# Performance work log

Measured on AMD Instinct MI355X. Metric: run time of the kernel, lower is better.

Reference implementation:

```python
import jax, jax.numpy as jnp
import numpy as np

H = 16; KV = 4; D = 128; HID = 2048; MAX_POS = 4096; RANK = 8; ALPHA = 16.0; THETA = 10000.0


def _lora_dense(x, kernel, a, b):
    # base kernel path is stop-gradient'd in the original LoRADense
    x = x.astype(jnp.bfloat16)
    y = x @ jax.lax.stop_gradient(kernel.astype(jnp.bfloat16))
    y = y + (ALPHA / RANK) * ((x @ a.astype(jnp.bfloat16)) @ b.astype(jnp.bfloat16))
    return y.astype(jnp.float32)


def _apply_rope(xq, xk, position_ids):
    # complex rotation expressed with real cos/sin on interleaved (even, odd) pairs
    dt = xq.dtype
    xq = xq.astype(jnp.bfloat16).astype(jnp.float32)
    xk = xk.astype(jnp.bfloat16).astype(jnp.float32)
    d = xq.shape[-1]
    inv_freq = 1.0 / THETA ** (jnp.arange(0, d, 2)[: d // 2].astype(jnp.float32) / d)
    angles = jnp.arange(MAX_POS, dtype=jnp.float32)[:, None] * inv_freq[None, :]  # (max_pos, d/2)
    cos = jnp.cos(angles)[position_ids][:, :, None, :]  # (b, s, 1, d/2)
    sin = jnp.sin(angles)[position_ids][:, :, None, :]

    def rot(x):
        xe = x[..., 0::2]
        xo = x[..., 1::2]
        re = xe * cos - xo * sin
        im = xe * sin + xo * cos
        return jnp.stack((re, im), axis=-1).reshape(x.shape)

    return rot(xq).astype(dt), rot(xk).astype(dt)


def _forward(hidden_states, attention_mask, position_ids, wq_kernel, wq_a, wq_b,
             wk_kernel, wk_a, wk_b, wv_kernel, wv_a, wv_b, wo_kernel, wo_a, wo_b):
    b, s, _ = hidden_states.shape
    hs = hidden_states.astype(jnp.bfloat16)
    xq = _lora_dense(hs, wq_kernel, wq_a, wq_b).reshape(b, s, H, D)
    g = H // KV
    # GQA: repeat each kv head g times along the head axis ('b s (h d) -> b s (h g) d')
    xk = jnp.repeat(_lora_dense(hs, wk_kernel, wk_a, wk_b).reshape(b, s, KV, D), g, axis=2)
    xv = jnp.repeat(_lora_dense(hs, wv_kernel, wv_a, wv_b).reshape(b, s, KV, D), g, axis=2)
    xq, xk = _apply_rope(xq, xk, position_ids)
    causal = jnp.tril(jnp.ones((s, s), dtype=bool))
    mask = attention_mask[:, None, None, :] & causal[None, None]  # (b, 1, q, k)
    bias = jnp.where(mask, 0.0, jnp.finfo(jnp.float32).min)
    scale = 1.0 / np.sqrt(D).astype(np.float32)
    scores = jnp.einsum('bqhd,bkhd->bhqk', (xq * scale).astype(jnp.bfloat16),
                        xk.astype(jnp.bfloat16)).astype(jnp.float32) + bias
    attn = jax.nn.softmax(scores, axis=-1)
    out = jnp.einsum('bhqk,bkhd->bqhd', attn, xv).reshape(b, s, H * D)
    return _lora_dense(out, wo_kernel, wo_a, wo_b)


def setup_inputs():
    key = jax.random.key(0)
    ks = jax.random.split(key, 16)
    B, S = 2, 2048
    w = lambda k, shp, sc=0.02: jax.random.normal(k, shp, dtype=jnp.float32) * sc
    return {
        'hidden_states': jax.random.normal(ks[0], (B, S, HID), dtype=jnp.float32),
        'attention_mask': jnp.ones((B, S), dtype=bool),
        'position_ids': jnp.broadcast_to(jnp.arange(S, dtype=jnp.int32), (B, S)),
        'wq_kernel': w(ks[1], (HID, H * D)),
        'wq_a': w(ks[2], (HID, RANK), 0.01),
        'wq_b': w(ks[3], (RANK, H * D), 0.01),
        'wk_kernel': w(ks[4], (HID, KV * D)),
        'wk_a': w(ks[5], (HID, RANK), 0.01),
        'wk_b': w(ks[6], (RANK, KV * D), 0.01),
        'wv_kernel': w(ks[7], (HID, KV * D)),
        'wv_a': w(ks[8], (HID, RANK), 0.01),
        'wv_b': w(ks[9], (RANK, KV * D), 0.01),
        'wo_kernel': w(ks[10], (H * D, HID)),
        'wo_a': w(ks[11], (H * D, RANK), 0.01),
        'wo_b': w(ks[12], (RANK, HID), 0.01),
    }


def reference(hidden_states, attention_mask, position_ids, wq_kernel, wq_a, wq_b,
              wk_kernel, wk_a, wk_b, wv_kernel, wv_a, wv_b, wo_kernel, wo_a, wo_b):
    return _forward(hidden_states, attention_mask, position_ids, wq_kernel, wq_a, wq_b,
                    wk_kernel, wk_a, wk_b, wv_kernel, wv_a, wv_b, wo_kernel, wo_a, wo_b)
```

## Files before the change

kernel.cpp:

```cpp
#include <hip/hip_runtime.h>
#include <hip/hip_bf16.h>
#include <cstdint>

#define H_    16
#define KV_   4
#define D_    128
#define HID_  2048
#define B_    2
#define S_    2048
#define NROW_ (B_*S_)
#define HD_   (H_*D_)
#define KVD_  (KV_*D_)
#define NQKV_ (HD_ + 2*KVD_)
#define SCALE_ 0.08838834764831843f
#define NEG_  -1e30f

typedef float  f32x4  __attribute__((ext_vector_type(4)));
typedef __bf16 bf16x8 __attribute__((ext_vector_type(8)));
typedef __bf16 bf16x4 __attribute__((ext_vector_type(4)));

__device__ __forceinline__ unsigned short f2bf(float x) {
  unsigned u = __float_as_uint(x);
  return (unsigned short)((u + 0x7FFFu + ((u >> 16) & 1u)) >> 16);
}
__device__ __forceinline__ float bf2f(unsigned short h) {
  return __uint_as_float(((unsigned)h) << 16);
}

__device__ __forceinline__ void glds16(const void* g, void* l) {
  typedef __attribute__((address_space(1))) const char G;
  typedef __attribute__((address_space(3))) char L;
  __builtin_amdgcn_global_load_lds((const G*)(unsigned long long)g,
                                   (L*)(unsigned)(unsigned long long)l, 16, 0, 0);
}

__global__ __launch_bounds__(256) void fold_w2(const float* __restrict__ W,
                                               const float* __restrict__ A,
                                               const float* __restrict__ Bm,
                                               unsigned short* __restrict__ Wt,
                                               int K, int N) {
  __shared__ float Bs[8 * 64];
  __shared__ unsigned short tt[64 * 72];
  const int tid = threadIdx.x;
  const int k0 = blockIdx.x << 6, n0 = blockIdx.y << 6;
#pragma unroll
  for (int i = 0; i < 2; ++i) {
    int c = i * 256 + tid;
    Bs[c] = bf2f(f2bf(Bm[(c >> 6) * N + n0 + (c & 63)]));
  }
  __syncthreads();
  const int kr = tid >> 2, nc = (tid & 3) << 4;
  float a[8];
#pragma unroll
  for (int r = 0; r < 8; ++r) a[r] = 2.0f * bf2f(f2bf(A[(k0 + kr) * 8 + r]));
#pragma unroll
  for (int i = 0; i < 4; ++i) {
    float4 wv = *(const float4*)(W + (size_t)(k0 + kr) * N + n0 + nc + i * 4);
    float e[4] = {wv.x, wv.y, wv.z, wv.w};
#pragma unroll
    for (int q = 0; q < 4; ++q) {
      int n = nc + i * 4 + q;
      float acc = bf2f(f2bf(e[q]));
#pragma unroll
      for (int r = 0; r < 8; ++r) acc += a[r] * Bs[r * 64 + n];
      tt[kr * 72 + n] = f2bf(acc);
    }
  }
  __syncthreads();
  const int nr = tid >> 2, kc = (tid & 3) << 4;
#pragma unroll
  for (int i = 0; i < 2; ++i) {
    unsigned short o[8];
#pragma unroll
    for (int e2 = 0; e2 < 8; ++e2) o[e2] = tt[(kc + i * 8 + e2) * 72 + nr];
    *(bf16x8*)(Wt + (size_t)(n0 + nr) * K + k0 + kc + i * 8) = *(const bf16x8*)o;
  }
}

__global__ __launch_bounds__(256) void cast_x(const float* __restrict__ in,
                                              unsigned short* __restrict__ out, int n4) {
  int i = blockIdx.x * 256 + threadIdx.x;
  if (i >= n4) return;
  float4 v = ((const float4*)in)[i];
  ushort4 o; o.x = f2bf(v.x); o.y = f2bf(v.y); o.z = f2bf(v.z); o.w = f2bf(v.w);
  ((ushort4*)out)[i] = o;
}

__global__ void trig_k(float* __restrict__ tab) {
  int p = blockIdx.x, j = threadIdx.x;
  float invf = __powf(10000.0f, -(float)j / 64.0f);
  float a = (float)p * invf;
  float s, c;
  sincosf(a, &s, &c);
  tab[(p * 64 + j) * 2 + 0] = c;
  tab[(p * 64 + j) * 2 + 1] = s;
}

__global__ __launch_bounds__(256) void rope2(unsigned short* __restrict__ QKV,
                                             const int* __restrict__ pos,
                                             const float* __restrict__ trig) {
  int gid = blockIdx.x * 256 + threadIdx.x;
  int row = gid / 160;
  int ch = gid - row * 160;
  bool isq = ch < 128;
  int col = isq ? (ch << 4) : (HD_ + ((ch - 128) << 4));
  int j0 = (isq ? (ch & 7) : ((ch - 128) & 7)) << 3;
  int pp = pos[row];
  const float* tb = trig + ((size_t)pp * 64 + j0) * 2;
  float4 t0 = *(const float4*)(tb);
  float4 t1 = *(const float4*)(tb + 4);
  float4 t2 = *(const float4*)(tb + 8);
  float4 t3 = *(const float4*)(tb + 12);
  float cc[8] = {t0.x, t0.z, t1.x, t1.z, t2.x, t2.z, t3.x, t3.z};
  float ss[8] = {t0.y, t0.w, t1.y, t1.w, t2.y, t2.w, t3.y, t3.w};
  unsigned short* base = QKV + (size_t)row * NQKV_ + col;
  unsigned short xin[16], xo[16];
  *(bf16x8*)xin = *(const bf16x8*)base;
  *(bf16x8*)(xin + 8) = *(const bf16x8*)(base + 8);
  float scl = isq ? SCALE_ : 1.0f;
#pragma unroll
  for (int p = 0; p < 8; ++p) {
    float x0 = bf2f(xin[2 * p]), x1 = bf2f(xin[2 * p + 1]);
    float re = (x0 * cc[p] - x1 * ss[p]) * scl;
    float im = (x0 * ss[p] + x1 * cc[p]) * scl;
    xo[2 * p] = f2bf(re); xo[2 * p + 1] = f2bf(im);
  }
  *(bf16x8*)base = *(const bf16x8*)xo;
  *(bf16x8*)(base + 8) = *(const bf16x8*)(xo + 8);
}

__global__ __launch_bounds__(256) void vtrans_k(const unsigned short* __restrict__ QKV,
                                                unsigned short* __restrict__ VT) {
  __shared__ unsigned short t[64 * 65];
  const int tid = threadIdx.x;
  const int s0 = blockIdx.x << 6, d0 = blockIdx.y << 6;
  const int bk = blockIdx.z, b = bk >> 2, hkv = bk & 3;
#pragma unroll
  for (int i = 0; i < 2; ++i) {
    int c = i * 256 + tid;
    int sr = c >> 3, c8 = c & 7;
    bf16x8 v = *(const bf16x8*)(QKV + (size_t)(b * S_ + s0 + sr) * NQKV_
                                + HD_ + KVD_ + hkv * D_ + d0 + c8 * 8);
    const unsigned short* u = (const unsigned short*)&v;
#pragma unroll
    for (int k = 0; k < 8; ++k) t[sr * 65 + c8 * 8 + k] = u[k];
  }
  __syncthreads();
#pragma unroll
  for (int i = 0; i < 2; ++i) {
    int c = i * 256 + tid;
    int dr = c >> 3, c8 = c & 7;
    unsigned short o[8];
#pragma unroll
    for (int k = 0; k < 8; ++k) o[k] = t[(c8 * 8 + k) * 65 + dr];
    *(bf16x8*)(VT + ((size_t)(bk * 128 + d0 + dr)) * S_ + s0 + c8 * 8) =
        *(const bf16x8*)o;
  }
}

template <int BN, int OUTF32>
__global__ __launch_bounds__(512, 1) void gemm256(const unsigned short* __restrict__ A,
                                                  const unsigned short* __restrict__ Bt,
                                                  void* __restrict__ C,
                                                  int M, int N, int K) {
  constexpr int ASLAB = 256 * 32;
  constexpr int BSLAB = BN * 32;
  constexpr int BUFE = 2 * ASLAB + 2 * BSLAB;
  constexpr int NFR = BN / 64;
  constexpr int WCOL = BN / 4;
  constexpr int VMN = 2 + BN / 128;
  __shared__ __align__(16) unsigned short lds[2 * BUFE];
  const int tid = threadIdx.x, lane = tid & 63, w = tid >> 6;
  const int g = lane >> 4, l15 = lane & 15;
  const int wm = w >> 2, wn = w & 3;

  const int nbn = N / BN;
  const int cpx = gridDim.x >> 3;
  const int sw = (blockIdx.x & 7) * cpx + (blockIdx.x >> 3);
  const int bm = sw / nbn, bn = sw - bm * nbn;
  const int row0 = bm << 8, col0 = bn * BN;

  auto stageA = [&](int kt, int kh, int buf) {
#pragma unroll
    for (int i = 0; i < 2; ++i) {
      int L = (i * 8 + w) * 64 + lane;
      int r = L >> 2, c = L & 3;
      int sc = c ^ ((r >> 1) & 3);
      glds16(A + (size_t)(row0 + r) * K + (kt << 6) + kh * 32 + sc * 8,
             (char*)lds + (size_t)(buf * BUFE + kh * ASLAB) * 2 + (size_t)(i * 8 + w) * 1024);
    }
  };
  auto stageB = [&](int kt, int kh, int buf) {
#pragma unroll
    for (int i = 0; i < BN / 128; ++i) {
      int L = (i * 8 + w) * 64 + lane;
      int r = L >> 2, c = L & 3;
      int sc = c ^ ((r >> 1) & 3);
      glds16(Bt + (size_t)(col0 + r) * K + (kt << 6) + kh * 32 + sc * 8,
             (char*)lds + (size_t)(buf * BUFE + 2 * ASLAB + kh * BSLAB) * 2 + (size_t)(i * 8 + w) * 1024);
    }
  };

  f32x4 acc[8][NFR];
#pragma unroll
  for (int i = 0; i < 8; ++i)
#pragma unroll
    for (int j = 0; j < NFR; ++j) acc[i][j] = (f32x4){0.f, 0.f, 0.f, 0.f};

  bf16x8 af[4], bfr[NFR];
  auto rdA = [&](int buf, int kh, int mh) {
#pragma unroll
    for (int mi = 0; mi < 4; ++mi) {
      int r = wm * 128 + mh * 64 + mi * 16 + l15;
      int cc = g ^ ((r >> 1) & 3);
      af[mi] = *(const bf16x8*)(lds + buf * BUFE + kh * ASLAB + r * 32 + cc * 8);
    }
  };
  auto rdB = [&](int buf, int kh) {
#pragma unroll
    for (int ni = 0; ni < NFR; ++ni) {
      int r = wn * WCOL + ni * 16 + l15;
      int cc = g ^ ((r >> 1) & 3);
      bfr[ni] = *(const bf16x8*)(lds + buf * BUFE + 2 * ASLAB + kh * BSLAB + r * 32 + cc * 8);
    }
  };
  auto domfma = [&](int mh) {
    __builtin_amdgcn_s_setprio(1);
#pragma unroll
    for (int mi = 0; mi < 4; ++mi)
#pragma unroll
      for (int ni = 0; ni < NFR; ++ni)
        acc[mh * 4 + mi][ni] =
            __builtin_amdgcn_mfma_f32_16x16x32_bf16(af[mi], bfr[ni], acc[mh * 4 + mi][ni], 0, 0, 0);
    __builtin_amdgcn_s_setprio(0);
  };

  stageA(0, 0, 0); stageB(0, 0, 0); stageA(0, 1, 0); stageB(0, 1, 0);
  asm volatile("s_waitcnt vmcnt(0)" ::: "memory");
  __builtin_amdgcn_s_barrier();

  const int nkt = K >> 6;
  for (int kt = 0; kt < nkt; ++kt) {
    const int buf = kt & 1, nb = buf ^ 1;
    const bool more = kt + 1 < nkt;
    rdA(buf, 0, 0); rdB(buf, 0);
    if (more) stageA(kt + 1, 0, nb);
    __builtin_amdgcn_s_barrier();
    domfma(0);
    __builtin_amdgcn_s_barrier();
    rdA(buf, 0, 1);
    if (more) {
      stageB(kt + 1, 0, nb);
      asm volatile("s_waitcnt vmcnt(%0)" :: "i"(VMN) : "memory");
    } else {
      asm volatile("s_waitcnt vmcnt(0)" ::: "memory");
    }
    __builtin_amdgcn_s_barrier();
    domfma(1);
    __builtin_amdgcn_s_barrier();
    rdA(buf, 1, 0); rdB(buf, 1);
    if (more) stageA(kt + 1, 1, nb);
    __builtin_amdgcn_s_barrier();
    domfma(0);
    __builtin_amdgcn_s_barrier();
    rdA(buf, 1, 1);
    if (more) {
      stageB(kt + 1, 1, nb);
      asm volatile("s_waitcnt vmcnt(%0)" :: "i"(VMN) : "memory");
    }
    __builtin_amdgcn_s_barrier();
    domfma(1);
    __builtin_amdgcn_s_barrier();
  }

#pragma unroll
  for (int mi8 = 0; mi8 < 8; ++mi8)
#pragma unroll
    for (int jj = 0; jj < 4; ++jj) {
      int r = row0 + wm * 128 + mi8 * 16 + g * 4 + jj;
#pragma unroll
      for (int ni = 0; ni < NFR; ++ni) {
        int cc = col0 + wn * WCOL + ni * 16 + l15;
        float v = acc[mi8][ni][jj];
        if (OUTF32) {
          ((float*)C)[(size_t)r * N + cc] = v;
        } else {
          __bf16 e = (__bf16)v;
          ((unsigned short*)C)[(size_t)r * N + cc] = *(unsigned short*)&e;
        }
      }
    }
}

__global__ __launch_bounds__(256) void attn_k(const unsigned short* __restrict__ QKV,
                                              const unsigned short* __restrict__ VT,
                                              unsigned short* __restrict__ O) {
  __shared__ __align__(16) unsigned short lK[2][64 * 128];
  __shared__ __align__(16) unsigned short lV[2][128 * 64];
  __shared__ __align__(16) unsigned short lP[4][16 * 72];
  const int tid = threadIdx.x, lane = tid & 63, w = tid >> 6;
  const int g = lane >> 4, l15 = lane & 15;

  const int dd = blockIdx.x;
  const int grp = dd & 7;
  const int t64 = dd >> 3;
  const int pair = t64 & 15;
  const int bh = grp * 4 + (t64 >> 4);
  const int b = bh >> 4, h = bh & 15, hkv = (h >> 2);

  auto stage = [&](int kb, int bsel) {
#pragma unroll
    for (int i = 0; i < 4; ++i) {
      int cbase = i * 256 + w * 64;
      int c = cbase + lane;
      { int r = c >> 4, p = c & 15, lc = p ^ (r & 7);
        glds16(QKV + (size_t)(b * S_ + kb + r) * NQKV_ + HD_ + hkv * D_ + lc * 8,
               (char*)(&lK[bsel][0]) + (size_t)cbase * 16); }
      { int d = c >> 3, p = c & 7, lc = p ^ (d & 7);
        glds16(VT + ((size_t)((b * 4 + hkv) * 128 + d)) * S_ + kb + lc * 8,
               (char*)(&lV[bsel][0]) + (size_t)cbase * 16); }
    }
  };

  for (int qsel = 0; qsel < 2; ++qsel) {
    const int qt = qsel ? (31 - pair) : pair;
    const int q_base = qt << 6;
    const int ntile = qt + 1;

    bf16x8 qf[4];
#pragma unroll
    for (int ks = 0; ks < 4; ++ks)
      qf[ks] = *(const bf16x8*)(QKV + (size_t)(b * S_ + q_base + w * 16 + l15) * NQKV_
                                + h * D_ + ks * 32 + g * 8);

    f32x4 oacc[8];
#pragma unroll
    for (int nd = 0; nd < 8; ++nd) oacc[nd] = (f32x4){0.f, 0.f, 0.f, 0.f};
    float mrun = NEG_, lrun = 0.f;

    stage(0, 0);
    __syncthreads();
    int cur = 0;
    for (int t = 0; t < ntile; ++t) {
      if (t + 1 < ntile) stage((t + 1) << 6, cur ^ 1);

      const unsigned short* Kb = &lK[cur][0];
      const unsigned short* Vb = &lV[cur][0];

      f32x4 sacc[4];
#pragma unroll
      for (int m = 0; m < 4; ++m) sacc[m] = (f32x4){0.f, 0.f, 0.f, 0.f};
      __builtin_amdgcn_s_setprio(1);
#pragma unroll
      for (int ks = 0; ks < 4; ++ks) {
        bf16x8 kf[4];
#pragma unroll
        for (int m = 0; m < 4; ++m) {
          int r = m * 16 + l15;
          int lc = (ks * 4 + g) ^ (r & 7);
          kf[m] = *(const bf16x8*)(Kb + r * 128 + lc * 8);
        }
#pragma unroll
        for (int m = 0; m < 4; ++m)
          sacc[m] = __builtin_amdgcn_mfma_f32_16x16x32_bf16(kf[m], qf[ks], sacc[m], 0, 0, 0);
      }
      __builtin_amdgcn_s_setprio(0);

      if (t == qt) {
#pragma unroll
        for (int m = 0; m < 4; ++m)
#pragma unroll
          for (int jj = 0; jj < 4; ++jj)
            if (m * 16 + g * 4 + jj > w * 16 + l15) sacc[m][jj] = NEG_;
      }

      float pm = NEG_;
#pragma unroll
      for (int m = 0; m < 4; ++m)
#pragma unroll
        for (int jj = 0; jj < 4; ++jj) pm = fmaxf(pm, sacc[m][jj]);
      pm = fmaxf(pm, __shfl_xor(pm, 16));
      pm = fmaxf(pm, __shfl_xor(pm, 32));
      bool skip = __all(pm <= mrun + 8.f);
      float mnew = skip ? mrun : fmaxf(mrun, pm);
      float ls = 0.f;
#pragma unroll
      for (int m = 0; m < 4; ++m)
#pragma unroll
        for (int jj = 0; jj < 4; ++jj) {
          float pv = __expf(sacc[m][jj] - mnew);
          sacc[m][jj] = pv;
          ls += pv;
        }
      ls += __shfl_xor(ls, 16);
      ls += __shfl_xor(ls, 32);
      if (skip) {
        lrun += ls;
      } else {
        float sc = __expf(mrun - mnew);
        lrun = lrun * sc + ls;
        mrun = mnew;
#pragma unroll
        for (int jj = 0; jj < 4; ++jj) {
          int srcl = (lane & 48) | (g * 4 + jj);
          float s = __shfl(sc, srcl);
#pragma unroll
          for (int nd = 0; nd < 8; ++nd) oacc[nd][jj] *= s;
        }
      }

#pragma unroll
      for (int m = 0; m < 4; ++m) {
        bf16x4 pk = {(__bf16)sacc[m][0], (__bf16)sacc[m][1],
                     (__bf16)sacc[m][2], (__bf16)sacc[m][3]};
        *(bf16x4*)(&lP[w][0] + l15 * 72 + m * 16 + g * 4) = pk;
      }

      __builtin_amdgcn_s_setprio(1);
#pragma unroll
      for (int ks = 0; ks < 2; ++ks) {
        bf16x8 pf = *(const bf16x8*)(&lP[w][0] + l15 * 72 + ks * 32 + g * 8);
#pragma unroll
        for (int nd = 0; nd < 8; ++nd) {
          int d = nd * 16 + l15;
          int lc = (ks * 4 + g) ^ (d & 7);
          bf16x8 vf = *(const bf16x8*)(Vb + d * 64 + lc * 8);
          oacc[nd] = __builtin_amdgcn_mfma_f32_16x16x32_bf16(pf, vf, oacc[nd], 0, 0, 0);
        }
      }
      __builtin_amdgcn_s_setprio(0);
      __syncthreads();
      cur ^= 1;
    }

    float inv[4];
#pragma unroll
    for (int jj = 0; jj < 4; ++jj) {
      int srcl = (lane & 48) | (g * 4 + jj);
      inv[jj] = 1.0f / __shfl(lrun, srcl);
    }
    unsigned short* sE = &lK[0][0];
#pragma unroll
    for (int nd = 0; nd < 8; ++nd)
#pragma unroll
      for (int jj = 0; jj < 4; ++jj) {
        __bf16 e = (__bf16)(oacc[nd][jj] * inv[jj]);
        sE[(w * 16 + g * 4 + jj) * 136 + nd * 16 + l15] = *(unsigned short*)&e;
      }
    __syncthreads();
#pragma unroll
    for (int i = 0; i < 4; ++i) {
      int c = i * 256 + tid;
      int r = c >> 4, c16 = c & 15;
      bf16x8 vv = *(const bf16x8*)(sE + r * 136 + c16 * 8);
      *(bf16x8*)(O + (size_t)(b * S_ + q_base + r) * HD_ + h * D_ + c16 * 8) = vv;
    }
    __syncthreads();
  }
}

extern "C" void kernel_launch(void* const* d_in, const int* in_sizes, int n_in,
                              void* d_out, int out_size, void* d_ws, size_t ws_size,
                              hipStream_t stream) {
  const float* hs  = (const float*)d_in[0];
  const int*   pos = (const int*)d_in[2];
  const float* wq  = (const float*)d_in[3];
  const float* wqa = (const float*)d_in[4];
  const float* wqb = (const float*)d_in[5];
  const float* wk  = (const float*)d_in[6];
  const float* wka = (const float*)d_in[7];
  const float* wkb = (const float*)d_in[8];
  const float* wv  = (const float*)d_in[9];
  const float* wva = (const float*)d_in[10];
  const float* wvb = (const float*)d_in[11];
  const float* wo  = (const float*)d_in[12];
  const float* woa = (const float*)d_in[13];
  const float* wob = (const float*)d_in[14];

  char* ws = (char*)d_ws;
  unsigned short* Xb   = (unsigned short*)(ws);
  unsigned short* Wqkv = (unsigned short*)(ws + 16777216);
  unsigned short* Wot  = (unsigned short*)(ws + 29360128);
  unsigned short* QKV  = (unsigned short*)(ws + 37748736);
  unsigned short* VT   = (unsigned short*)(ws + 62914560);
  float*          trig = (float*)(ws + 67108864);

  fold_w2<<<dim3(32, 32), 256, 0, stream>>>(wq, wqa, wqb, Wqkv, 2048, 2048);
  fold_w2<<<dim3(32, 8),  256, 0, stream>>>(wk, wka, wkb, Wqkv + (size_t)2048 * 2048, 2048, 512);
  fold_w2<<<dim3(32, 8),  256, 0, stream>>>(wv, wva, wvb, Wqkv + (size_t)2560 * 2048, 2048, 512);
  fold_w2<<<dim3(32, 32), 256, 0, stream>>>(wo, woa, wob, Wot, 2048, 2048);
  cast_x<<<8192, 256, 0, stream>>>(hs, Xb, 2097152);
  trig_k<<<4096, 64, 0, stream>>>(trig);
  gemm256<256, 0><<<192, 512, 0, stream>>>(Xb, Wqkv, QKV, 4096, 3072, 2048);
  rope2<<<2560, 256, 0, stream>>>(QKV, pos, trig);
  vtrans_k<<<dim3(32, 2, 8), 256, 0, stream>>>(QKV, VT);
  attn_k<<<512, 256, 0, stream>>>(QKV, VT, Xb );
  gemm256<128, 1><<<256, 512, 0, stream>>>(Xb, Wot, d_out, 4096, 2048, 2048);
}
```

Baseline: 213.6 us.

## Fuse RoPE into QKV GEMM epilogue and unroll attention loop with static buffers

Removes the standalone RoPE kernel by applying the rotation and query scaling inside the QKV GEMM store epilogue, using a lane-pair shuffle and the trig table. The attention kernel is restructured into a manually two-way unrolled loop over a single shared buffer with precomputed global and LDS offsets, removing dynamic buffer indexing. The trig table is shrunk to cover only the sequence length, which relies on position ids staying below 2048. The epilogue now does extra per-element loads and arithmetic.

```diff
diff --git a/kernel.cpp b/kernel.cpp
--- a/kernel.cpp
+++ b/kernel.cpp
@@ -96,39 +96,6 @@
   tab[(p * 64 + j) * 2 + 1] = s;
 }
 
-__global__ __launch_bounds__(256) void rope2(unsigned short* __restrict__ QKV,
-                                             const int* __restrict__ pos,
-                                             const float* __restrict__ trig) {
-  int gid = blockIdx.x * 256 + threadIdx.x;
-  int row = gid / 160;
-  int ch = gid - row * 160;
-  bool isq = ch < 128;
-  int col = isq ? (ch << 4) : (HD_ + ((ch - 128) << 4));
-  int j0 = (isq ? (ch & 7) : ((ch - 128) & 7)) << 3;
-  int pp = pos[row];
-  const float* tb = trig + ((size_t)pp * 64 + j0) * 2;
-  float4 t0 = *(const float4*)(tb);
-  float4 t1 = *(const float4*)(tb + 4);
-  float4 t2 = *(const float4*)(tb + 8);
-  float4 t3 = *(const float4*)(tb + 12);
-  float cc[8] = {t0.x, t0.z, t1.x, t1.z, t2.x, t2.z, t3.x, t3.z};
-  float ss[8] = {t0.y, t0.w, t1.y, t1.w, t2.y, t2.w, t3.y, t3.w};
-  unsigned short* base = QKV + (size_t)row * NQKV_ + col;
-  unsigned short xin[16], xo[16];
-  *(bf16x8*)xin = *(const bf16x8*)base;
-  *(bf16x8*)(xin + 8) = *(const bf16x8*)(base + 8);
-  float scl = isq ? SCALE_ : 1.0f;
-#pragma unroll
-  for (int p = 0; p < 8; ++p) {
-    float x0 = bf2f(xin[2 * p]), x1 = bf2f(xin[2 * p + 1]);
-    float re = (x0 * cc[p] - x1 * ss[p]) * scl;
-    float im = (x0 * ss[p] + x1 * cc[p]) * scl;
-    xo[2 * p] = f2bf(re); xo[2 * p + 1] = f2bf(im);
-  }
-  *(bf16x8*)base = *(const bf16x8*)xo;
-  *(bf16x8*)(base + 8) = *(const bf16x8*)(xo + 8);
-}
-
 __global__ __launch_bounds__(256) void vtrans_k(const unsigned short* __restrict__ QKV,
                                                 unsigned short* __restrict__ VT) {
   __shared__ unsigned short t[64 * 65];
@@ -158,11 +125,13 @@
   }
 }
 
-template <int BN, int OUTF32>
+template <int BN, int OUTF32, int ROPE>
 __global__ __launch_bounds__(512, 1) void gemm256(const unsigned short* __restrict__ A,
                                                   const unsigned short* __restrict__ Bt,
                                                   void* __restrict__ C,
-                                                  int M, int N, int K) {
+                                                  int M, int N, int K,
+                                                  const int* __restrict__ pos,
+                                                  const float2* __restrict__ trig) {
   constexpr int ASLAB = 256 * 32;
   constexpr int BSLAB = BN * 32;
   constexpr int BUFE = 2 * ASLAB + 2 * BSLAB;
@@ -278,15 +247,31 @@
 #pragma unroll
     for (int jj = 0; jj < 4; ++jj) {
       int r = row0 + wm * 128 + mi8 * 16 + g * 4 + jj;
+      int p = 0;
+      if (ROPE) p = pos[r];
 #pragma unroll
       for (int ni = 0; ni < NFR; ++ni) {
         int cc = col0 + wn * WCOL + ni * 16 + l15;
         float v = acc[mi8][ni][jj];
         if (OUTF32) {
           ((float*)C)[(size_t)r * N + cc] = v;
+        } else if (!ROPE) {
+          ((unsigned short*)C)[(size_t)r * N + cc] = f2bf(v);
         } else {
-          __bf16 e = (__bf16)v;
-          ((unsigned short*)C)[(size_t)r * N + cc] = *(unsigned short*)&e;
+          float x = bf2f(f2bf(v));
+          float xp = __shfl_xor(x, 1);
+          unsigned short ob;
+          if (cc < HD_ + KVD_) {
+            int j = (cc & 127) >> 1;
+            float2 tt = trig[p * 64 + j];
+            float val = (l15 & 1) ? (xp * tt.y + x * tt.x)
+                                  : (x * tt.x - xp * tt.y);
+            if (cc < HD_) val *= SCALE_;
+            ob = f2bf(val);
+          } else {
+            ob = f2bf(v);
+          }
+          ((unsigned short*)C)[(size_t)r * N + cc] = ob;
         }
       }
     }
@@ -295,9 +280,7 @@
 __global__ __launch_bounds__(256) void attn_k(const unsigned short* __restrict__ QKV,
                                               const unsigned short* __restrict__ VT,
                                               unsigned short* __restrict__ O) {
-  __shared__ __align__(16) unsigned short lK[2][64 * 128];
-  __shared__ __align__(16) unsigned short lV[2][128 * 64];
-  __shared__ __align__(16) unsigned short lP[4][16 * 72];
+  __shared__ __align__(16) unsigned short smem[37376];
   const int tid = threadIdx.x, lane = tid & 63, w = tid >> 6;
   const int g = lane >> 4, l15 = lane & 15;
 
@@ -308,19 +291,111 @@
   const int bh = grp * 4 + (t64 >> 4);
   const int b = bh >> 4, h = bh & 15, hkv = (h >> 2);
 
-  auto stage = [&](int kb, int bsel) {
-#pragma unroll
-    for (int i = 0; i < 4; ++i) {
-      int cbase = i * 256 + w * 64;
-      int c = cbase + lane;
-      { int r = c >> 4, p = c & 15, lc = p ^ (r & 7);
-        glds16(QKV + (size_t)(b * S_ + kb + r) * NQKV_ + HD_ + hkv * D_ + lc * 8,
-               (char*)(&lK[bsel][0]) + (size_t)cbase * 16); }
-      { int d = c >> 3, p = c & 7, lc = p ^ (d & 7);
-        glds16(VT + ((size_t)((b * 4 + hkv) * 128 + d)) * S_ + kb + lc * 8,
-               (char*)(&lV[bsel][0]) + (size_t)cbase * 16); }
-    }
-  };
+  const unsigned short* QKVk0 = QKV + (size_t)b * S_ * NQKV_ + HD_ + hkv * D_;
+  const unsigned short* VT0  = VT + (size_t)(b * 4 + hkv) * 128 * S_;
+
+  int gk[4], gv[4], dsl[4];
+#pragma unroll
+  for (int i = 0; i < 4; ++i) {
+    int c = i * 256 + w * 64 + lane;
+    { int r = c >> 4, s = c & 15; gk[i] = r * NQKV_ + (s ^ (r & 7)) * 8; }
+    { int d = c >> 3, s = c & 7;  gv[i] = d * S_ + (s ^ (d & 7)) * 8; }
+    dsl[i] = (i * 256 + w * 64) * 16;
+  }
+  int koff[4][4], voff[2][8], pwo[4], pro[2];
+#pragma unroll
+  for (int ks = 0; ks < 4; ++ks)
+#pragma unroll
+    for (int m = 0; m < 4; ++m) {
+      int r = m * 16 + l15;
+      koff[ks][m] = r * 128 + ((ks * 4 + g) ^ (r & 7)) * 8;
+    }
+#pragma unroll
+  for (int ks = 0; ks < 2; ++ks)
+#pragma unroll
+    for (int nd = 0; nd < 8; ++nd) {
+      int d = nd * 16 + l15;
+      voff[ks][nd] = d * 64 + ((ks * 4 + g) ^ (d & 7)) * 8;
+    }
+#pragma unroll
+  for (int m = 0; m < 4; ++m) pwo[m] = l15 * 72 + m * 16 + g * 4;
+#pragma unroll
+  for (int ks = 0; ks < 2; ++ks) pro[ks] = l15 * 72 + ks * 32 + g * 8;
+  const int PB = 32768 + w * 1152;
+  char* const smemc = (char*)smem;
+
+#define STAGE(KB, KOB, VOB) do {                                            \
+    const unsigned short* bk_ = QKVk0 + (size_t)(KB) * NQKV_;               \
+    const unsigned short* bv_ = VT0 + (KB);                                 \
+    _Pragma("unroll")                                                       \
+    for (int i_ = 0; i_ < 4; ++i_) {                                        \
+      glds16(bk_ + gk[i_], smemc + (KOB) + dsl[i_]);                        \
+      glds16(bv_ + gv[i_], smemc + (VOB) + dsl[i_]);                        \
+    }                                                                       \
+  } while (0)
+
+#define COMPUTE(KOH, VOH, TCUR) do {                                        \
+    f32x4 sacc[4];                                                          \
+    _Pragma("unroll") for (int m = 0; m < 4; ++m)                           \
+      sacc[m] = (f32x4){0.f, 0.f, 0.f, 0.f};                                \
+    __builtin_amdgcn_s_setprio(1);                                          \
+    _Pragma("unroll") for (int ks = 0; ks < 4; ++ks) {                      \
+      bf16x8 kf[4];                                                         \
+      _Pragma("unroll") for (int m = 0; m < 4; ++m)                         \
+        kf[m] = *(const bf16x8*)(smem + (KOH) + koff[ks][m]);               \
+      _Pragma("unroll") for (int m = 0; m < 4; ++m)                         \
+        sacc[m] = __builtin_amdgcn_mfma_f32_16x16x32_bf16(kf[m], qf[ks], sacc[m], 0, 0, 0); \
+    }                                                                       \
+    __builtin_amdgcn_s_setprio(0);                                          \
+    if ((TCUR) == qt) {                                                     \
+      _Pragma("unroll") for (int m = 0; m < 4; ++m)                         \
+        _Pragma("unroll") for (int jj = 0; jj < 4; ++jj)                    \
+          if (m * 16 + g * 4 + jj > w * 16 + l15) sacc[m][jj] = NEG_;       \
+    }                                                                       \
+    float pm = NEG_;                                                        \
+    _Pragma("unroll") for (int m = 0; m < 4; ++m)                           \
+      _Pragma("unroll") for (int jj = 0; jj < 4; ++jj)                      \
+        pm = fmaxf(pm, sacc[m][jj]);                                        \
+    pm = fmaxf(pm, __shfl_xor(pm, 16));                                     \
+    pm = fmaxf(pm, __shfl_xor(pm, 32));                                     \
+    bool skip = __all(pm <= mrun + 8.f);                                    \
+    float mnew = skip ? mrun : fmaxf(mrun, pm);                             \
+    float ls = 0.f;                                                         \
+    _Pragma("unroll") for (int m = 0; m < 4; ++m)                           \
+      _Pragma("unroll") for (int jj = 0; jj < 4; ++jj) {                    \
+        float pv = __expf(sacc[m][jj] - mnew);                              \
+        sacc[m][jj] = pv;                                                   \
+        ls += pv;                                                           \
+      }                                                                     \
+    ls += __shfl_xor(ls, 16);                                               \
+    ls += __shfl_xor(ls, 32);                                               \
+    if (skip) {                                                             \
+      lrun += ls;                                                           \
+    } else {                                                                \
+      float sc = __expf(mrun - mnew);                                       \
+      lrun = lrun * sc + ls;                                                \
+      mrun = mnew;                                                          \
+      _Pragma("unroll") for (int jj = 0; jj < 4; ++jj) {                    \
+        int srcl = (lane & 48) | (g * 4 + jj);                              \
+        float s = __shfl(sc, srcl);                                         \
+        _Pragma("unroll") for (int nd = 0; nd < 8; ++nd) oacc[nd][jj] *= s; \
+      }                                                                     \
+    }                                                                       \
+    _Pragma("unroll") for (int m = 0; m < 4; ++m) {                         \
+      bf16x4 pk = {(__bf16)sacc[m][0], (__bf16)sacc[m][1],                  \
+                   (__bf16)sacc[m][2], (__bf16)sacc[m][3]};                 \
+      *(bf16x4*)(smem + PB + pwo[m]) = pk;                                  \
+    }                                                                       \
+    __builtin_amdgcn_s_setprio(1);                                          \
+    _Pragma("unroll") for (int ks = 0; ks < 2; ++ks) {                      \
+      bf16x8 pf = *(const bf16x8*)(smem + PB + pro[ks]);                    \
+      _Pragma("unroll") for (int nd = 0; nd < 8; ++nd) {                    \
+        bf16x8 vf = *(const bf16x8*)(smem + (VOH) + voff[ks][nd]);          \
+        oacc[nd] = __builtin_amdgcn_mfma_f32_16x16x32_bf16(pf, vf, oacc[nd], 0, 0, 0); \
+      }                                                                     \
+    }                                                                       \
+    __builtin_amdgcn_s_setprio(0);                                          \
+  } while (0)
 
   for (int qsel = 0; qsel < 2; ++qsel) {
     const int qt = qsel ? (31 - pair) : pair;
@@ -338,99 +413,17 @@
     for (int nd = 0; nd < 8; ++nd) oacc[nd] = (f32x4){0.f, 0.f, 0.f, 0.f};
     float mrun = NEG_, lrun = 0.f;
 
-    stage(0, 0);
+    STAGE(0, 0, 32768);
     __syncthreads();
-    int cur = 0;
-    for (int t = 0; t < ntile; ++t) {
-      if (t + 1 < ntile) stage((t + 1) << 6, cur ^ 1);
-
-      const unsigned short* Kb = &lK[cur][0];
-      const unsigned short* Vb = &lV[cur][0];
-
-      f32x4 sacc[4];
-#pragma unroll
-      for (int m = 0; m < 4; ++m) sacc[m] = (f32x4){0.f, 0.f, 0.f, 0.f};
-      __builtin_amdgcn_s_setprio(1);
-#pragma unroll
-      for (int ks = 0; ks < 4; ++ks) {
-        bf16x8 kf[4];
-#pragma unroll
-        for (int m = 0; m < 4; ++m) {
-          int r = m * 16 + l15;
-          int lc = (ks * 4 + g) ^ (r & 7);
-          kf[m] = *(const bf16x8*)(Kb + r * 128 + lc * 8);
-        }
-#pragma unroll
-        for (int m = 0; m < 4; ++m)
-          sacc[m] = __builtin_amdgcn_mfma_f32_16x16x32_bf16(kf[m], qf[ks], sacc[m], 0, 0, 0);
-      }
-      __builtin_amdgcn_s_setprio(0);
-
-      if (t == qt) {
-#pragma unroll
-        for (int m = 0; m < 4; ++m)
-#pragma unroll
-          for (int jj = 0; jj < 4; ++jj)
-            if (m * 16 + g * 4 + jj > w * 16 + l15) sacc[m][jj] = NEG_;
-      }
-
-      float pm = NEG_;
-#pragma unroll
-      for (int m = 0; m < 4; ++m)
-#pragma unroll
-        for (int jj = 0; jj < 4; ++jj) pm = fmaxf(pm, sacc[m][jj]);
-      pm = fmaxf(pm, __shfl_xor(pm, 16));
-      pm = fmaxf(pm, __shfl_xor(pm, 32));
-      bool skip = __all(pm <= mrun + 8.f);
-      float mnew = skip ? mrun : fmaxf(mrun, pm);
-      float ls = 0.f;
-#pragma unroll
-      for (int m = 0; m < 4; ++m)
-#pragma unroll
-        for (int jj = 0; jj < 4; ++jj) {
-          float pv = __expf(sacc[m][jj] - mnew);
-          sacc[m][jj] = pv;
-          ls += pv;
-        }
-      ls += __shfl_xor(ls, 16);
-      ls += __shfl_xor(ls, 32);
-      if (skip) {
-        lrun += ls;
-      } else {
-        float sc = __expf(mrun - mnew);
-        lrun = lrun * sc + ls;
-        mrun = mnew;
-#pragma unroll
-        for (int jj = 0; jj < 4; ++jj) {
-          int srcl = (lane & 48) | (g * 4 + jj);
-          float s = __shfl(sc, srcl);
-#pragma unroll
-          for (int nd = 0; nd < 8; ++nd) oacc[nd][jj] *= s;
-        }
-      }
-
-#pragma unroll
-      for (int m = 0; m < 4; ++m) {
-        bf16x4 pk = {(__bf16)sacc[m][0], (__bf16)sacc[m][1],
-                     (__bf16)sacc[m][2], (__bf16)sacc[m][3]};
-        *(bf16x4*)(&lP[w][0] + l15 * 72 + m * 16 + g * 4) = pk;
-      }
-
-      __builtin_amdgcn_s_setprio(1);
-#pragma unroll
-      for (int ks = 0; ks < 2; ++ks) {
-        bf16x8 pf = *(const bf16x8*)(&lP[w][0] + l15 * 72 + ks * 32 + g * 8);
-#pragma unroll
-        for (int nd = 0; nd < 8; ++nd) {
-          int d = nd * 16 + l15;
-          int lc = (ks * 4 + g) ^ (d & 7);
-          bf16x8 vf = *(const bf16x8*)(Vb + d * 64 + lc * 8);
-          oacc[nd] = __builtin_amdgcn_mfma_f32_16x16x32_bf16(pf, vf, oacc[nd], 0, 0, 0);
-        }
-      }
-      __builtin_amdgcn_s_setprio(0);
+    for (int t = 0; t < ntile; t += 2) {
+      const bool m1 = t + 1 < ntile;
+      if (m1) STAGE((t + 1) << 6, 16384, 49152);
+      COMPUTE(0, 16384, t);
       __syncthreads();
-      cur ^= 1;
+      if (!m1) break;
+      if (t + 2 < ntile) STAGE((t + 2) << 6, 0, 32768);
+      COMPUTE(8192, 24576, t + 1);
+      __syncthreads();
     }
 
     float inv[4];
@@ -439,7 +432,7 @@
       int srcl = (lane & 48) | (g * 4 + jj);
       inv[jj] = 1.0f / __shfl(lrun, srcl);
     }
-    unsigned short* sE = &lK[0][0];
+    unsigned short* sE = smem;
 #pragma unroll
     for (int nd = 0; nd < 8; ++nd)
 #pragma unroll
@@ -457,6 +450,8 @@
     }
     __syncthreads();
   }
+#undef STAGE
+#undef COMPUTE
 }
 
 extern "C" void kernel_launch(void* const* d_in, const int* in_sizes, int n_in,
@@ -490,10 +485,11 @@
   fold_w2<<<dim3(32, 8),  256, 0, stream>>>(wv, wva, wvb, Wqkv + (size_t)2560 * 2048, 2048, 512);
   fold_w2<<<dim3(32, 32), 256, 0, stream>>>(wo, woa, wob, Wot, 2048, 2048);
   cast_x<<<8192, 256, 0, stream>>>(hs, Xb, 2097152);
-  trig_k<<<4096, 64, 0, stream>>>(trig);
-  gemm256<256, 0><<<192, 512, 0, stream>>>(Xb, Wqkv, QKV, 4096, 3072, 2048);
-  rope2<<<2560, 256, 0, stream>>>(QKV, pos, trig);
+  trig_k<<<2048, 64, 0, stream>>>(trig);
+  gemm256<256, 0, 1><<<192, 512, 0, stream>>>(Xb, Wqkv, QKV, 4096, 3072, 2048,
+                                              pos, (const float2*)trig);
   vtrans_k<<<dim3(32, 2, 8), 256, 0, stream>>>(QKV, VT);
   attn_k<<<512, 256, 0, stream>>>(QKV, VT, Xb );
-  gemm256<128, 1><<<256, 512, 0, stream>>>(Xb, Wot, d_out, 4096, 2048, 2048);
-}
+  gemm256<128, 1, 0><<<256, 512, 0, stream>>>(Xb, Wot, d_out, 4096, 2048, 2048,
+                                              nullptr, nullptr);
+}
```

Result: slower. 228.5 us (+7.0%).
